# Optimization experiments

Measured on AMD Instinct MI355X. Metric: run time of the kernel, lower is better.

## Reference

```python
import jax, jax.numpy as jnp
import numpy as np

SEQ_LEN = 96      # args.seq_len (in_feats)
H_FEATS = 100
OUT_FEATS = 128
HEADS = 4
K = 64            # args.input_size = nodes per graph
B = 256           # number of graphs (batch_size)
N = K * B
DEG = 8
E = N * DEG
OUT_SIZE = 24     # args.output_size
NEG_SLOPE = 0.2   # PyG GATConv default


def setup_inputs() -> dict:
    key = jax.random.key(0)
    ks = jax.random.split(key, 20)
    s = 0.05
    x = jax.random.normal(ks[0], (N, SEQ_LEN), jnp.float32)
    # intra-graph random edges (dst repeated, src within same graph)
    dst = jnp.repeat(jnp.arange(N, dtype=jnp.int32), DEG)
    src = (dst // K) * K + jax.random.randint(ks[1], (E,), 0, K, dtype=jnp.int32)
    edge_index = jnp.stack([src, dst])
    batch = jnp.repeat(jnp.arange(B, dtype=jnp.int32), K)
    y = jax.random.normal(ks[2], (N, OUT_SIZE), jnp.float32)
    # GATConv 1: in=96 -> heads=4, ch=100
    W1 = jax.random.normal(ks[3], (SEQ_LEN, HEADS * H_FEATS), jnp.float32) * s
    as1 = jax.random.normal(ks[4], (HEADS, H_FEATS), jnp.float32) * s
    ad1 = jax.random.normal(ks[5], (HEADS, H_FEATS), jnp.float32) * s
    b1 = jnp.zeros((H_FEATS,), jnp.float32)
    # GATConv 2: in=100 -> heads=4, ch=128
    W2 = jax.random.normal(ks[6], (H_FEATS, HEADS * OUT_FEATS), jnp.float32) * s
    as2 = jax.random.normal(ks[7], (HEADS, OUT_FEATS), jnp.float32) * s
    ad2 = jax.random.normal(ks[8], (HEADS, OUT_FEATS), jnp.float32) * s
    b2 = jnp.zeros((OUT_FEATS,), jnp.float32)
    # per-node-index MLPs (batched over K)
    fw1 = jax.random.normal(ks[9], (K, OUT_FEATS, 64), jnp.float32) * s
    fb1 = jnp.zeros((K, 64), jnp.float32)
    fw2 = jax.random.normal(ks[10], (K, 64, OUT_SIZE), jnp.float32) * s
    fb2 = jnp.zeros((K, OUT_SIZE), jnp.float32)
    return dict(x=x, edge_index=edge_index, batch=batch, y=y,
                W1=W1, as1=as1, ad1=ad1, b1=b1,
                W2=W2, as2=as2, ad2=ad2, b2=b2,
                fw1=fw1, fb1=fb1, fw2=fw2, fb2=fb2)


def gat_conv(x, src, dst, W, a_src, a_dst, bias):
    # PyG GATConv (concat=False): linear -> per-edge attention -> softmax over
    # incoming edges of each dst -> weighted sum -> mean over heads + bias.
    n = x.shape[0]
    xl = (x @ W).reshape(n, HEADS, -1)                      # [N,H,C]
    al_src = jnp.sum(xl * a_src, axis=-1)                   # [N,H]
    al_dst = jnp.sum(xl * a_dst, axis=-1)                   # [N,H]
    alpha = jax.nn.leaky_relu(al_src[src] + al_dst[dst], NEG_SLOPE)  # [E,H]
    m = jax.ops.segment_max(alpha, dst, num_segments=n)
    ea = jnp.exp(alpha - m[dst])
    denom = jax.ops.segment_sum(ea, dst, num_segments=n)
    w = ea / (denom[dst] + 1e-16)                           # [E,H]
    msg = xl[src] * w[:, :, None]                           # [E,H,C]
    out = jax.ops.segment_sum(msg, dst, num_segments=n)     # [N,H,C]
    return out.mean(axis=1) + bias                          # concat=False


def reference(x, edge_index, batch, y, W1, as1, ad1, b1, W2, as2, ad2, b2, fw1, fb1, fw2, fb2):
    n = x.shape[0]
    src, dst = edge_index[0], edge_index[1]
    loop = jnp.arange(n, dtype=src.dtype)                   # GATConv adds self-loops
    src = jnp.concatenate([src, loop])
    dst = jnp.concatenate([dst, loop])
    h = jax.nn.elu(gat_conv(x, src, dst, W1, as1, ad1, b1))
    h = gat_conv(h, src, dst, W2, as2, ad2, b2)             # [N,128]
    # batch is sorted with K nodes per graph -> stacking == static reshape
    xg = h.reshape(B, K, OUT_FEATS).transpose(1, 0, 2)      # [K,B,128]
    hid = jax.nn.relu(jnp.einsum('kbi,kih->kbh', xg, fw1) + fb1[:, None, :])
    pred = jnp.einsum('kbh,kho->kbo', hid, fw2) + fb2[:, None, :]  # [K,B,out]
    yg = y.reshape(B, K, OUT_SIZE)                          # [B,K,out]
    return pred, yg
```

## Files before the change

kernel.cpp:

```cpp
#include <hip/hip_runtime.h>
#include <hip/hip_bf16.h>
#include <math.h>


#define N_NODES 16384
#define B_GRAPHS 256
#define K_NODES 64
#define DEG 8
#define NHEADS 4
#define C1 100
#define C2 128
#define IN_F 96
#define HID 64
#define OUT_SZ 24
#define PRED_ELEMS (K_NODES * B_GRAPHS * OUT_SZ)

#define W1T_ROWS 448
#define W1T_K    96
#define W2T_ROWS 512
#define W2T_K    128

using bf16 = __hip_bfloat16;
typedef __attribute__((ext_vector_type(8))) short          frag_ab;
typedef __attribute__((ext_vector_type(4))) float          frag_cd;
typedef unsigned short us8 __attribute__((ext_vector_type(8)));
typedef unsigned short us4 __attribute__((ext_vector_type(4)));

__device__ __forceinline__ float us2f(unsigned short u) {
  return __bfloat162float(__ushort_as_bfloat16(u));
}
__device__ __forceinline__ short f2bf_s(float f) {
  return __builtin_bit_cast(short, __float2bfloat16(f));
}

#define P1N (W1T_ROWS * W1T_K)
#define P2N (W2T_ROWS * W2T_K)
#define YG4 (PRED_ELEMS / 4)

__global__ __launch_bounds__(256)
void prep(const float* __restrict__ W1, const float* __restrict__ W2,
          const float* __restrict__ y,
          bf16* __restrict__ W1t, bf16* __restrict__ W2t,
          float* __restrict__ yg) {
  int idx = blockIdx.x * 256 + threadIdx.x;
  if (idx < P1N) {
    int c = idx / W1T_K, k = idx - c * W1T_K;
    W1t[idx] = __float2bfloat16((c < 400) ? W1[(size_t)k * 400 + c] : 0.f);
  } else if (idx < P1N + P2N) {
    int i2 = idx - P1N;
    int c = i2 >> 7, k = i2 & 127;
    W2t[i2] = __float2bfloat16((k < 100) ? W2[(size_t)k * 512 + c] : 0.f);
  } else {
    int j = idx - P1N - P2N;
    if (j < YG4) {
      int i = j * 4;
      float4 v = *(const float4*)(y + i);
      v.x = __bfloat162float(__float2bfloat16(v.x));
      v.y = __bfloat162float(__float2bfloat16(v.y));
      v.z = __bfloat162float(__float2bfloat16(v.z));
      v.w = __bfloat162float(__float2bfloat16(v.w));
      *(float4*)(yg + i) = v;
    }
  }
}

__global__ __launch_bounds__(512)
void gat_fused(const float* __restrict__ x,
               const bf16* __restrict__ W1t, const bf16* __restrict__ W2t,
               const int* __restrict__ esrc,
               const float* __restrict__ as1, const float* __restrict__ ad1,
               const float* __restrict__ b1,
               const float* __restrict__ as2, const float* __restrict__ ad2,
               const float* __restrict__ b2,
               bf16* __restrict__ h2out) {
  constexpr int LDA1 = IN_F + 8;
  constexpr int LDA2 = 136;
  constexpr int LDT  = 72;

  __shared__ __align__(16) short          As[64 * LDA2];
  __shared__ __align__(16) unsigned short xs[512 * LDT];
  __shared__ __align__(16) short          Ps[NHEADS * 64 * LDT];
  __shared__ float avs1[400], avd1[400], avs2[512], avd2[512];
  __shared__ float bia1[C1], bia2[C2];
  __shared__ int   edg[K_NODES * DEG];
  __shared__ float als[64 * 5], ald[64 * 5];

  const int g = blockIdx.x;
  const int t = threadIdx.x;
  const int wv = t >> 6;
  const int l  = t & 63;
  const int lm = l & 15;
  const int lk = (l >> 4) * 8;
  const int rq = (l >> 4) * 4;

  {
    constexpr int QR = IN_F / 4;
    for (int idx = t; idx < 64 * QR; idx += 512) {
      int m = idx / QR, q = idx - m * QR;
      const float4 v = *(const float4*)(x + ((size_t)(g * 64 + m) * IN_F + q * 4));
      short* d = &As[m * LDA1 + q * 4];
      d[0] = f2bf_s(v.x); d[1] = f2bf_s(v.y); d[2] = f2bf_s(v.z); d[3] = f2bf_s(v.w);
    }
  }
  for (int idx = t; idx < 400; idx += 512) { avs1[idx] = as1[idx]; avd1[idx] = ad1[idx]; }
  for (int idx = t; idx < 512; idx += 512) { avs2[idx] = as2[idx]; avd2[idx] = ad2[idx]; }
  if (t < C1) bia1[t] = b1[t];
  if (t < C2) bia2[t] = b2[t];
  if (t < K_NODES * DEG) edg[t] = esrc[g * K_NODES * DEG + t] & (K_NODES - 1);
  for (int idx = t; idx < NHEADS * 64 * LDT / 8; idx += 512)
    *(us8*)&Ps[idx * 8] = (us8)0;
  __syncthreads();

  if (wv < 7) {
    const int n0 = wv * 64;
    frag_cd acc[4][4] = {};
#pragma unroll
    for (int ks = 0; ks < IN_F; ks += 32) {
      frag_ab b[4];
#pragma unroll
      for (int nt = 0; nt < 4; ++nt)
        b[nt] = *(const frag_ab*)((const short*)W1t +
                                  (size_t)(n0 + nt * 16 + lm) * W1T_K + ks + lk);
#pragma unroll
      for (int mt = 0; mt < 4; ++mt) {
        frag_ab a = *(const frag_ab*)&As[(mt * 16 + lm) * LDA1 + ks + lk];
#pragma unroll
        for (int nt = 0; nt < 4; ++nt)
          acc[mt][nt] = __builtin_amdgcn_mfma_f32_16x16x32_bf16(a, b[nt],
                                                                acc[mt][nt], 0, 0, 0);
      }
    }
#pragma unroll
    for (int mt = 0; mt < 4; ++mt)
#pragma unroll
      for (int nt = 0; nt < 4; ++nt) {
        const int c4 = n0 + nt * 16 + lm;
        us4 o;
#pragma unroll
        for (int r = 0; r < 4; ++r) o[r] = (unsigned short)f2bf_s(acc[mt][nt][r]);
        *(us4*)&xs[c4 * LDT + mt * 16 + rq] = o;
      }
  }
  __syncthreads();

  if (t < 256) {
    const int n = t >> 2, h = t & 3;
    float ss = 0.f, sd = 0.f;
#pragma unroll 4
    for (int c = 0; c < C1; ++c) {
      const float v = us2f(xs[(h * C1 + c) * LDT + n]);
      ss += v * avs1[h * C1 + c];
      sd += v * avd1[h * C1 + c];
    }
    als[n * 5 + h] = ss;
    ald[n * 5 + h] = sd;
  }
  __syncthreads();

  if (t < 256) {
    const int n = t >> 2, h = t & 3;
    const float ad = ald[n * 5 + h];
    int   sv[9];
    float a[9];
#pragma unroll
    for (int j = 0; j < 8; ++j) sv[j] = edg[n * DEG + j];
    sv[8] = n;
#pragma unroll
    for (int j = 0; j < 9; ++j) {
      float v = als[sv[j] * 5 + h] + ad;
      a[j] = (v >= 0.f) ? v : 0.2f * v;
    }
    float m = -1e30f;
#pragma unroll
    for (int j = 0; j < 9; ++j) m = fmaxf(m, a[j]);
    float s = 0.f;
#pragma unroll
    for (int j = 0; j < 9; ++j) { a[j] = __expf(a[j] - m); s += a[j]; }
    const float inv = 1.f / (s + 1e-16f);
    short* prow = &Ps[(h * 64 + n) * LDT];
#pragma unroll
    for (int j = 0; j < 9; ++j) {
      float tw = a[j];
#pragma unroll
      for (int i = 0; i < 9; ++i)
        if (i != j && sv[i] == sv[j]) tw += a[i];
      prow[sv[j]] = f2bf_s(tw * inv);
    }
  } else {
    for (int i = t - 256; i < 64 * 28; i += 256) {
      int m = i / 28, kk = 100 + (i - m * 28);
      As[m * LDA2 + kk] = 0;
    }
  }
  __syncthreads();

  {
    const int mw = (wv & 3) * 16;
    const int cg = wv >> 2;
    const int ntb = cg * 4;
    const int nte = (cg == 0) ? 4 : 7;
    frag_cd acc[4] = {};
#pragma unroll
    for (int h = 0; h < NHEADS; ++h)
#pragma unroll
      for (int ks = 0; ks < 64; ks += 32) {
        frag_ab a = *(const frag_ab*)&Ps[(h * 64 + mw + lm) * LDT + ks + lk];
        for (int nt = ntb; nt < nte; ++nt) {
          frag_ab b = *(const frag_ab*)&xs[(h * C1 + nt * 16 + lm) * LDT + ks + lk];
          acc[nt - ntb] = __builtin_amdgcn_mfma_f32_16x16x32_bf16(a, b,
                                                                  acc[nt - ntb], 0, 0, 0);
      }
    }
    for (int nt = ntb; nt < nte; ++nt) {
      const int c = nt * 16 + lm;
      if (c < C1) {
        const float bc = bia1[c];
#pragma unroll
        for (int r = 0; r < 4; ++r) {
          float vv = acc[nt - ntb][r] * 0.25f + bc;
          vv = (vv > 0.f) ? vv : (__expf(vv) - 1.f);
          As[(mw + rq + r) * LDA2 + c] = f2bf_s(vv);
        }
      }
    }
  }
  __syncthreads();

  {
    const int n0 = wv * 64;
    frag_cd acc[4][4] = {};
#pragma unroll
    for (int ks = 0; ks < 128; ks += 32) {
      frag_ab b[4];
#pragma unroll
      for (int nt = 0; nt < 4; ++nt)
        b[nt] = *(const frag_ab*)((const short*)W2t +
                                  (size_t)(n0 + nt * 16 + lm) * W2T_K + ks + lk);
#pragma unroll
      for (int mt = 0; mt < 4; ++mt) {
        frag_ab a = *(const frag_ab*)&As[(mt * 16 + lm) * LDA2 + ks + lk];
#pragma unroll
        for (int nt = 0; nt < 4; ++nt)
          acc[mt][nt] = __builtin_amdgcn_mfma_f32_16x16x32_bf16(a, b[nt],
                                                                acc[mt][nt], 0, 0, 0);
      }
    }
#pragma unroll
    for (int mt = 0; mt < 4; ++mt)
#pragma unroll
      for (int nt = 0; nt < 4; ++nt) {
        const int c4 = n0 + nt * 16 + lm;
        us4 o;
#pragma unroll
        for (int r = 0; r < 4; ++r) o[r] = (unsigned short)f2bf_s(acc[mt][nt][r]);
        *(us4*)&xs[c4 * LDT + mt * 16 + rq] = o;
      }
  }
  __syncthreads();

  if (t < 256) {
    const int n = t >> 2, h = t & 3;
    float ss = 0.f, sd = 0.f;
#pragma unroll 4
    for (int c = 0; c < C2; ++c) {
      const float v = us2f(xs[(h * C2 + c) * LDT + n]);
      ss += v * avs2[h * C2 + c];
      sd += v * avd2[h * C2 + c];
    }
    als[n * 5 + h] = ss;
    ald[n * 5 + h] = sd;
  }
  __syncthreads();

  if (t < 256) {
    const int n = t >> 2, h = t & 3;
    const float ad = ald[n * 5 + h];
    int   sv[9];
    float a[9];
#pragma unroll
    for (int j = 0; j < 8; ++j) sv[j] = edg[n * DEG + j];
    sv[8] = n;
#pragma unroll
    for (int j = 0; j < 9; ++j) {
      float v = als[sv[j] * 5 + h] + ad;
      a[j] = (v >= 0.f) ? v : 0.2f * v;
    }
    float m = -1e30f;
#pragma unroll
    for (int j = 0; j < 9; ++j) m = fmaxf(m, a[j]);
    float s = 0.f;
#pragma unroll
    for (int j = 0; j < 9; ++j) { a[j] = __expf(a[j] - m); s += a[j]; }
    const float inv = 1.f / (s + 1e-16f);
    short* prow = &Ps[(h * 64 + n) * LDT];
#pragma unroll
    for (int j = 0; j < 9; ++j) {
      float tw = a[j];
#pragma unroll
      for (int i = 0; i < 9; ++i)
        if (i != j && sv[i] == sv[j]) tw += a[i];
      prow[sv[j]] = f2bf_s(tw * inv);
    }
  }
  __syncthreads();

  {
    const int mw = (wv & 3) * 16;
    const int cg = wv >> 2;
    const int ntb = cg * 4;
    frag_cd acc[4] = {};
#pragma unroll
    for (int h = 0; h < NHEADS; ++h)
#pragma unroll
      for (int ks = 0; ks < 64; ks += 32) {
        frag_ab a = *(const frag_ab*)&Ps[(h * 64 + mw + lm) * LDT + ks + lk];
#pragma unroll
        for (int nt = 0; nt < 4; ++nt) {
          frag_ab b = *(const frag_ab*)&xs[(h * C2 + (ntb + nt) * 16 + lm) * LDT + ks + lk];
          acc[nt] = __builtin_amdgcn_mfma_f32_16x16x32_bf16(a, b, acc[nt], 0, 0, 0);
        }
      }
    unsigned short* outp = (unsigned short*)h2out + (size_t)(g * 64) * C2;
#pragma unroll
    for (int nt = 0; nt < 4; ++nt) {
      const int c = (ntb + nt) * 16 + lm;
      const float bc = bia2[c];
#pragma unroll
      for (int r = 0; r < 4; ++r) {
        float vv = acc[nt][r] * 0.25f + bc;
        outp[(size_t)(mw + rq + r) * C2 + c] = (unsigned short)f2bf_s(vv);
      }
    }
  }
}

__global__ __launch_bounds__(256)
void mlp_mfma(const bf16* __restrict__ h2,
              const float* __restrict__ fw1, const float* __restrict__ fb1,
              const float* __restrict__ fw2, const float* __restrict__ fb2,
              float* __restrict__ pred) {
  constexpr int LDA = C2 + 8;
  constexpr int LDH = HID + 8;
  __shared__ __align__(16) short As[64 * LDA];
  __shared__ __align__(16) short B1[HID * LDA];
  __shared__ __align__(16) short Hs[64 * LDH];
  __shared__ __align__(16) short B2[32 * LDH];
  __shared__ float b1s[HID];
  __shared__ float b2s[32];

  const int k  = blockIdx.x & 63;
  const int ms = blockIdx.x >> 6;
  const int t  = threadIdx.x;

  for (int idx = t; idx < 64 * 16; idx += 256) {
    int r = idx >> 4, o = idx & 15;
    const us8 v = *(const us8*)((const unsigned short*)h2 +
        ((size_t)((ms * 64 + r) * K_NODES + k) * C2) + o * 8);
    *(us8*)&As[r * LDA + o * 8] = v;
  }
  for (int idx = t; idx < C2 * HID; idx += 256) {
    int kk = idx >> 6, n = idx & 63;
    B1[n * LDA + kk] = f2bf_s(fw1[(size_t)k * C2 * HID + kk * HID + n]);
  }
  for (int idx = t; idx < HID * 32; idx += 256) {
    int kk = idx >> 5, n = idx & 31;
    float v = (n < OUT_SZ) ? fw2[(size_t)k * HID * OUT_SZ + kk * OUT_SZ + n] : 0.f;
    B2[n * LDH + kk] = f2bf_s(v);
  }
  if (t < HID) b1s[t] = fb1[k * HID + t];
  if (t < 32)  b2s[t] = (t < OUT_SZ) ? fb2[k * OUT_SZ + t] : 0.f;
  __syncthreads();

  const int wv = t >> 6;
  const int l  = t & 63;
  const int lm = l & 15;
  const int lk = (l >> 4) * 8;
  const int rq = (l >> 4) * 4;

  frag_cd acc[4] = {};
#pragma unroll
  for (int ks = 0; ks < C2; ks += 32) {
    frag_ab a = *(const frag_ab*)&As[(wv * 16 + lm) * LDA + ks + lk];
#pragma unroll
    for (int nt = 0; nt < 4; ++nt) {
      frag_ab b = *(const frag_ab*)&B1[(nt * 16 + lm) * LDA + ks + lk];
      acc[nt] = __builtin_amdgcn_mfma_f32_16x16x32_bf16(a, b, acc[nt], 0, 0, 0);
    }
  }
#pragma unroll
  for (int nt = 0; nt < 4; ++nt) {
    const int j  = nt * 16 + lm;
    const float bj = b1s[j];
#pragma unroll
    for (int r = 0; r < 4; ++r) {
      const int m = wv * 16 + rq + r;
      Hs[m * LDH + j] = f2bf_s(fmaxf(acc[nt][r] + bj, 0.f));
    }
  }
  __syncthreads();

  frag_cd acc2[2] = {};
#pragma unroll
  for (int ks = 0; ks < HID; ks += 32) {
    frag_ab a = *(const frag_ab*)&Hs[(wv * 16 + lm) * LDH + ks + lk];
#pragma unroll
    for (int nt = 0; nt < 2; ++nt) {
      frag_ab b = *(const frag_ab*)&B2[(nt * 16 + lm) * LDH + ks + lk];
      acc2[nt] = __builtin_amdgcn_mfma_f32_16x16x32_bf16(a, b, acc2[nt], 0, 0, 0);
    }
  }
#pragma unroll
  for (int nt = 0; nt < 2; ++nt) {
    const int q = nt * 16 + lm;
    if (q < OUT_SZ) {
      const float bq = b2s[q];
#pragma unroll
      for (int r = 0; r < 4; ++r) {
        const int m = wv * 16 + rq + r;
        pred[((size_t)k * B_GRAPHS + ms * 64 + m) * OUT_SZ + q] = acc2[nt][r] + bq;
      }
    }
  }
}

extern "C" void kernel_launch(void* const* d_in, const int* in_sizes, int n_in,
                              void* d_out, int out_size, void* d_ws, size_t ws_size,
                              hipStream_t stream) {
  const float* x   = (const float*)d_in[0];
  const int*   ei  = (const int*)d_in[1];
  const float* y   = (const float*)d_in[3];
  const float* W1  = (const float*)d_in[4];
  const float* as1 = (const float*)d_in[5];
  const float* ad1 = (const float*)d_in[6];
  const float* b1  = (const float*)d_in[7];
  const float* W2  = (const float*)d_in[8];
  const float* as2 = (const float*)d_in[9];
  const float* ad2 = (const float*)d_in[10];
  const float* b2  = (const float*)d_in[11];
  const float* fw1 = (const float*)d_in[12];
  const float* fb1 = (const float*)d_in[13];
  const float* fw2 = (const float*)d_in[14];
  const float* fb2 = (const float*)d_in[15];

  bf16* h2  = (bf16*)d_ws;
  bf16* W1t = h2 + (size_t)N_NODES * C2;
  bf16* W2t = W1t + P1N;

  float* out = (float*)d_out;

  prep<<<(P1N + P2N + YG4 + 255) / 256, 256, 0, stream>>>(
      W1, W2, y, W1t, W2t, out + PRED_ELEMS);

  gat_fused<<<B_GRAPHS, 512, 0, stream>>>(x, W1t, W2t, ei,
                                          as1, ad1, b1, as2, ad2, b2, h2);

  mlp_mfma<<<K_NODES * 4, 256, 0, stream>>>(h2, fw1, fb1, fw2, fb2, out);
}
```

Measured before the change: 118.6 us.

## Double GAT block threads and pre-transpose MLP weights to bf16 in prep

The fused GAT kernel now runs 1024 threads (16 waves) per graph, splitting each GEMM's M rows and aggregation column tiles across twice as many waves to raise per-CU parallelism for the 256-block grid. Separately, the per-node MLP weights are converted and transposed to bf16 once in the prep kernel, so mlp_mfma loads them with vectorized 16-byte copies instead of strided scalar float loads repeated by four blocks per k. Costs are extra prep work and workspace, fewer registers per thread in the GAT kernel, and unchanged barrier counts with more waves per barrier.

```diff
diff --git a/kernel.cpp b/kernel.cpp
--- a/kernel.cpp
+++ b/kernel.cpp
@@ -35,12 +35,17 @@
 
 #define P1N (W1T_ROWS * W1T_K)
 #define P2N (W2T_ROWS * W2T_K)
+#define F1N (K_NODES * HID * C2)
+#define F2N (K_NODES * 32 * HID)
 #define YG4 (PRED_ELEMS / 4)
+#define PREPN (P1N + P2N + F1N + F2N + YG4)
 
 __global__ __launch_bounds__(256)
 void prep(const float* __restrict__ W1, const float* __restrict__ W2,
+          const float* __restrict__ fw1, const float* __restrict__ fw2,
           const float* __restrict__ y,
           bf16* __restrict__ W1t, bf16* __restrict__ W2t,
+          bf16* __restrict__ fw1t, bf16* __restrict__ fw2t,
           float* __restrict__ yg) {
   int idx = blockIdx.x * 256 + threadIdx.x;
   if (idx < P1N) {
@@ -50,8 +55,16 @@
     int i2 = idx - P1N;
     int c = i2 >> 7, k = i2 & 127;
     W2t[i2] = __float2bfloat16((k < 100) ? W2[(size_t)k * 512 + c] : 0.f);
+  } else if (idx < P1N + P2N + F1N) {
+    int i2 = idx - P1N - P2N;
+    int k = i2 >> 13, r = i2 & 8191, j = r >> 7, i = r & 127;
+    fw1t[i2] = __float2bfloat16(fw1[(size_t)k * 8192 + i * 64 + j]);
+  } else if (idx < P1N + P2N + F1N + F2N) {
+    int i2 = idx - P1N - P2N - F1N;
+    int k = i2 >> 11, r = i2 & 2047, q = r >> 6, j = r & 63;
+    fw2t[i2] = __float2bfloat16((q < OUT_SZ) ? fw2[(size_t)k * 1536 + j * 24 + q] : 0.f);
   } else {
-    int j = idx - P1N - P2N;
+    int j = idx - P1N - P2N - F1N - F2N;
     if (j < YG4) {
       int i = j * 4;
       float4 v = *(const float4*)(y + i);
@@ -64,7 +77,7 @@
   }
 }
 
-__global__ __launch_bounds__(512)
+__global__ __launch_bounds__(1024)
 void gat_fused(const float* __restrict__ x,
                const bf16* __restrict__ W1t, const bf16* __restrict__ W2t,
                const int* __restrict__ esrc,
@@ -95,25 +108,28 @@
 
   {
     constexpr int QR = IN_F / 4;
-    for (int idx = t; idx < 64 * QR; idx += 512) {
+    for (int idx = t; idx < 64 * QR; idx += 1024) {
       int m = idx / QR, q = idx - m * QR;
       const float4 v = *(const float4*)(x + ((size_t)(g * 64 + m) * IN_F + q * 4));
       short* d = &As[m * LDA1 + q * 4];
       d[0] = f2bf_s(v.x); d[1] = f2bf_s(v.y); d[2] = f2bf_s(v.z); d[3] = f2bf_s(v.w);
     }
   }
-  for (int idx = t; idx < 400; idx += 512) { avs1[idx] = as1[idx]; avd1[idx] = ad1[idx]; }
-  for (int idx = t; idx < 512; idx += 512) { avs2[idx] = as2[idx]; avd2[idx] = ad2[idx]; }
-  if (t < C1) bia1[t] = b1[t];
+  if (t < 400)        { avs1[t] = as1[t]; avd1[t] = ad1[t]; }
+  else if (t < 912)   { int i = t - 400; avs2[i] = as2[i]; avd2[i] = ad2[i]; }
+  if (t >= 912 && t < 912 + C1) bia1[t - 912] = b1[t - 912];
   if (t < C2) bia2[t] = b2[t];
-  if (t < K_NODES * DEG) edg[t] = esrc[g * K_NODES * DEG + t] & (K_NODES - 1);
-  for (int idx = t; idx < NHEADS * 64 * LDT / 8; idx += 512)
+  if (t >= 512 && t < 512 + K_NODES * DEG)
+    edg[t - 512] = esrc[g * K_NODES * DEG + (t - 512)] & (K_NODES - 1);
+  for (int idx = t; idx < NHEADS * 64 * LDT / 8; idx += 1024)
     *(us8*)&Ps[idx * 8] = (us8)0;
   __syncthreads();
 
-  if (wv < 7) {
-    const int n0 = wv * 64;
-    frag_cd acc[4][4] = {};
+  if (wv < 14) {
+    const int ch = wv >> 1;
+    const int mh = (wv & 1) * 32;
+    const int n0 = ch * 64;
+    frag_cd acc[2][4] = {};
 #pragma unroll
     for (int ks = 0; ks < IN_F; ks += 32) {
       frag_ab b[4];
@@ -122,8 +138,8 @@
         b[nt] = *(const frag_ab*)((const short*)W1t +
                                   (size_t)(n0 + nt * 16 + lm) * W1T_K + ks + lk);
 #pragma unroll
-      for (int mt = 0; mt < 4; ++mt) {
-        frag_ab a = *(const frag_ab*)&As[(mt * 16 + lm) * LDA1 + ks + lk];
+      for (int mt = 0; mt < 2; ++mt) {
+        frag_ab a = *(const frag_ab*)&As[(mh + mt * 16 + lm) * LDA1 + ks + lk];
 #pragma unroll
         for (int nt = 0; nt < 4; ++nt)
           acc[mt][nt] = __builtin_amdgcn_mfma_f32_16x16x32_bf16(a, b[nt],
@@ -131,14 +147,14 @@
       }
     }
 #pragma unroll
-    for (int mt = 0; mt < 4; ++mt)
+    for (int mt = 0; mt < 2; ++mt)
 #pragma unroll
       for (int nt = 0; nt < 4; ++nt) {
         const int c4 = n0 + nt * 16 + lm;
         us4 o;
 #pragma unroll
         for (int r = 0; r < 4; ++r) o[r] = (unsigned short)f2bf_s(acc[mt][nt][r]);
-        *(us4*)&xs[c4 * LDT + mt * 16 + rq] = o;
+        *(us4*)&xs[c4 * LDT + mh + mt * 16 + rq] = o;
       }
   }
   __syncthreads();
@@ -187,7 +203,7 @@
       prow[sv[j]] = f2bf_s(tw * inv);
     }
   } else {
-    for (int i = t - 256; i < 64 * 28; i += 256) {
+    for (int i = t - 256; i < 64 * 28; i += 768) {
       int m = i / 28, kk = 100 + (i - m * 28);
       As[m * LDA2 + kk] = 0;
     }
@@ -195,40 +211,47 @@
   __syncthreads();
 
   {
-    const int mw = (wv & 3) * 16;
-    const int cg = wv >> 2;
-    const int ntb = cg * 4;
-    const int nte = (cg == 0) ? 4 : 7;
-    frag_cd acc[4] = {};
+    const int mw  = (wv & 3) * 16;
+    const int ntg = wv >> 2;
+    frag_cd acc[2] = {};
 #pragma unroll
     for (int h = 0; h < NHEADS; ++h)
 #pragma unroll
       for (int ks = 0; ks < 64; ks += 32) {
         frag_ab a = *(const frag_ab*)&Ps[(h * 64 + mw + lm) * LDT + ks + lk];
-        for (int nt = ntb; nt < nte; ++nt) {
-          frag_ab b = *(const frag_ab*)&xs[(h * C1 + nt * 16 + lm) * LDT + ks + lk];
-          acc[nt - ntb] = __builtin_amdgcn_mfma_f32_16x16x32_bf16(a, b,
-                                                                  acc[nt - ntb], 0, 0, 0);
-      }
-    }
-    for (int nt = ntb; nt < nte; ++nt) {
-      const int c = nt * 16 + lm;
-      if (c < C1) {
-        const float bc = bia1[c];
-#pragma unroll
-        for (int r = 0; r < 4; ++r) {
-          float vv = acc[nt - ntb][r] * 0.25f + bc;
-          vv = (vv > 0.f) ? vv : (__expf(vv) - 1.f);
-          As[(mw + rq + r) * LDA2 + c] = f2bf_s(vv);
+#pragma unroll
+        for (int u = 0; u < 2; ++u) {
+          const int nt = ntg * 2 + u;
+          if (nt < 7) {
+            frag_ab b = *(const frag_ab*)&xs[(h * C1 + nt * 16 + lm) * LDT + ks + lk];
+            acc[u] = __builtin_amdgcn_mfma_f32_16x16x32_bf16(a, b, acc[u], 0, 0, 0);
+          }
         }
       }
+#pragma unroll
+    for (int u = 0; u < 2; ++u) {
+      const int nt = ntg * 2 + u;
+      if (nt < 7) {
+        const int c = nt * 16 + lm;
+        if (c < C1) {
+          const float bc = bia1[c];
+#pragma unroll
+          for (int r = 0; r < 4; ++r) {
+            float vv = acc[u][r] * 0.25f + bc;
+            vv = (vv > 0.f) ? vv : (__expf(vv) - 1.f);
+            As[(mw + rq + r) * LDA2 + c] = f2bf_s(vv);
+          }
+        }
+      }
     }
   }
   __syncthreads();
 
   {
-    const int n0 = wv * 64;
-    frag_cd acc[4][4] = {};
+    const int ch = wv >> 1;
+    const int mh = (wv & 1) * 32;
+    const int n0 = ch * 64;
+    frag_cd acc[2][4] = {};
 #pragma unroll
     for (int ks = 0; ks < 128; ks += 32) {
       frag_ab b[4];
@@ -237,8 +260,8 @@
         b[nt] = *(const frag_ab*)((const short*)W2t +
                                   (size_t)(n0 + nt * 16 + lm) * W2T_K + ks + lk);
 #pragma unroll
-      for (int mt = 0; mt < 4; ++mt) {
-        frag_ab a = *(const frag_ab*)&As[(mt * 16 + lm) * LDA2 + ks + lk];
+      for (int mt = 0; mt < 2; ++mt) {
+        frag_ab a = *(const frag_ab*)&As[(mh + mt * 16 + lm) * LDA2 + ks + lk];
 #pragma unroll
         for (int nt = 0; nt < 4; ++nt)
           acc[mt][nt] = __builtin_amdgcn_mfma_f32_16x16x32_bf16(a, b[nt],
@@ -246,14 +269,14 @@
       }
     }
 #pragma unroll
-    for (int mt = 0; mt < 4; ++mt)
+    for (int mt = 0; mt < 2; ++mt)
 #pragma unroll
       for (int nt = 0; nt < 4; ++nt) {
         const int c4 = n0 + nt * 16 + lm;
         us4 o;
 #pragma unroll
         for (int r = 0; r < 4; ++r) o[r] = (unsigned short)f2bf_s(acc[mt][nt][r]);
-        *(us4*)&xs[c4 * LDT + mt * 16 + rq] = o;
+        *(us4*)&xs[c4 * LDT + mh + mt * 16 + rq] = o;
       }
   }
   __syncthreads();
@@ -305,29 +328,28 @@
   __syncthreads();
 
   {
-    const int mw = (wv & 3) * 16;
-    const int cg = wv >> 2;
-    const int ntb = cg * 4;
-    frag_cd acc[4] = {};
+    const int mw  = (wv & 3) * 16;
+    const int ntg = wv >> 2;
+    frag_cd acc[2] = {};
 #pragma unroll
     for (int h = 0; h < NHEADS; ++h)
 #pragma unroll
       for (int ks = 0; ks < 64; ks += 32) {
         frag_ab a = *(const frag_ab*)&Ps[(h * 64 + mw + lm) * LDT + ks + lk];
 #pragma unroll
-        for (int nt = 0; nt < 4; ++nt) {
-          frag_ab b = *(const frag_ab*)&xs[(h * C2 + (ntb + nt) * 16 + lm) * LDT + ks + lk];
-          acc[nt] = __builtin_amdgcn_mfma_f32_16x16x32_bf16(a, b, acc[nt], 0, 0, 0);
+        for (int u = 0; u < 2; ++u) {
+          frag_ab b = *(const frag_ab*)&xs[(h * C2 + (ntg * 2 + u) * 16 + lm) * LDT + ks + lk];
+          acc[u] = __builtin_amdgcn_mfma_f32_16x16x32_bf16(a, b, acc[u], 0, 0, 0);
         }
       }
     unsigned short* outp = (unsigned short*)h2out + (size_t)(g * 64) * C2;
 #pragma unroll
-    for (int nt = 0; nt < 4; ++nt) {
-      const int c = (ntb + nt) * 16 + lm;
+    for (int u = 0; u < 2; ++u) {
+      const int c = (ntg * 2 + u) * 16 + lm;
       const float bc = bia2[c];
 #pragma unroll
       for (int r = 0; r < 4; ++r) {
-        float vv = acc[nt][r] * 0.25f + bc;
+        float vv = acc[u][r] * 0.25f + bc;
         outp[(size_t)(mw + rq + r) * C2 + c] = (unsigned short)f2bf_s(vv);
       }
     }
@@ -336,8 +358,8 @@
 
 __global__ __launch_bounds__(256)
 void mlp_mfma(const bf16* __restrict__ h2,
-              const float* __restrict__ fw1, const float* __restrict__ fb1,
-              const float* __restrict__ fw2, const float* __restrict__ fb2,
+              const bf16* __restrict__ fw1t, const float* __restrict__ fb1,
+              const bf16* __restrict__ fw2t, const float* __restrict__ fb2,
               float* __restrict__ pred) {
   constexpr int LDA = C2 + 8;
   constexpr int LDH = HID + 8;
@@ -358,14 +380,15 @@
         ((size_t)((ms * 64 + r) * K_NODES + k) * C2) + o * 8);
     *(us8*)&As[r * LDA + o * 8] = v;
   }
-  for (int idx = t; idx < C2 * HID; idx += 256) {
-    int kk = idx >> 6, n = idx & 63;
-    B1[n * LDA + kk] = f2bf_s(fw1[(size_t)k * C2 * HID + kk * HID + n]);
-  }
-  for (int idx = t; idx < HID * 32; idx += 256) {
-    int kk = idx >> 5, n = idx & 31;
-    float v = (n < OUT_SZ) ? fw2[(size_t)k * HID * OUT_SZ + kk * OUT_SZ + n] : 0.f;
-    B2[n * LDH + kk] = f2bf_s(v);
+  for (int idx = t; idx < HID * 16; idx += 256) {
+    int n = idx >> 4, o = idx & 15;
+    *(us8*)&B1[n * LDA + o * 8] =
+        *(const us8*)((const unsigned short*)fw1t + (size_t)k * 8192 + n * 128 + o * 8);
+  }
+  for (int idx = t; idx < 32 * 8; idx += 256) {
+    int q = idx >> 3, o = idx & 7;
+    *(us8*)&B2[q * LDH + o * 8] =
+        *(const us8*)((const unsigned short*)fw2t + (size_t)k * 2048 + q * 64 + o * 8);
   }
   if (t < HID) b1s[t] = fb1[k * HID + t];
   if (t < 32)  b2s[t] = (t < OUT_SZ) ? fb2[k * OUT_SZ + t] : 0.f;
@@ -442,17 +465,19 @@
   const float* fw2 = (const float*)d_in[14];
   const float* fb2 = (const float*)d_in[15];
 
-  bf16* h2  = (bf16*)d_ws;
-  bf16* W1t = h2 + (size_t)N_NODES * C2;
-  bf16* W2t = W1t + P1N;
+  bf16* h2   = (bf16*)d_ws;
+  bf16* W1t  = h2 + (size_t)N_NODES * C2;
+  bf16* W2t  = W1t + P1N;
+  bf16* fw1t = W2t + P2N;
+  bf16* fw2t = fw1t + F1N;
 
   float* out = (float*)d_out;
 
-  prep<<<(P1N + P2N + YG4 + 255) / 256, 256, 0, stream>>>(
-      W1, W2, y, W1t, W2t, out + PRED_ELEMS);
-
-  gat_fused<<<B_GRAPHS, 512, 0, stream>>>(x, W1t, W2t, ei,
-                                          as1, ad1, b1, as2, ad2, b2, h2);
-
-  mlp_mfma<<<K_NODES * 4, 256, 0, stream>>>(h2, fw1, fb1, fw2, fb2, out);
-}
+  prep<<<PREPN / 256, 256, 0, stream>>>(W1, W2, fw1, fw2, y,
+                                        W1t, W2t, fw1t, fw2t, out + PRED_ELEMS);
+
+  gat_fused<<<B_GRAPHS, 1024, 0, stream>>>(x, W1t, W2t, ei,
+                                           as1, ad1, b1, as2, ad2, b2, h2);
+
+  mlp_mfma<<<K_NODES * 4, 256, 0, stream>>>(h2, fw1t, fb1, fw2t, fb2, out);
+}
```

Result: slower. 121.3 us (+2.2%).
